# Kernel tuning notes

Hardware: AMD Instinct MI355X
Metric: run time of the kernel (lower is better)

## Reference

```python
import jax, jax.numpy as jnp
import numpy as np

# db8 decomposition low-pass filter (pywt ordering, dec_lo)
_DB8_DEC_LO = np.array([
    -0.00011747678400228192, 0.0006754494059985568, -0.0003917403729959771,
    -0.00487035299301066, 0.008746094047015655, 0.013981027917015516,
    -0.04408825393106472, -0.01736930100202211, 0.128747426620186,
    0.00047248457399797254, -0.2840155429624281, -0.015829105256023893,
    0.5853546836548691, 0.6756307362980128, 0.3128715909144659,
    0.05441584224308161], dtype=np.float32)
_F = len(_DB8_DEC_LO)  # 16 taps
# quadrature mirror relation used by pywt: dec_hi[k] = (-1)^(k+1) * dec_lo[F-1-k]
_DB8_DEC_HI = (((-1.0) ** (np.arange(_F) + 1)) * _DB8_DEC_LO[::-1]).astype(np.float32)
# lax conv is cross-correlation; np.convolve flips the kernel -> pre-flip filters.
# Kernel layout [out_ch=2 (lo,hi), in_ch=1, width=F]
_KERNEL = jnp.asarray(np.stack([_DB8_DEC_LO[::-1], _DB8_DEC_HI[::-1]])[:, None, :])

WAVELET_LEVEL = 3
SPECTRAL_WEIGHT = 1.0
WAVELET_WEIGHT = 1.0


def _dwt_level(x):
    """Single-level db8 DWT with pywt 'symmetric' padding, batched over rows.

    x: [N, L] -> (cA, cD) each [N, (L + F - 1) // 2]
    Matches: np.convolve(sym_pad(x, F-1), dec_filter, 'valid')[1::2]
    """
    p = _F - 1
    # half-sample symmetric extension: [x_p..x_1 | x | x_{L-1}..x_{L-p}]
    xe = jnp.concatenate([x[:, :p][:, ::-1], x, x[:, -p:][:, ::-1]], axis=1)
    xe = xe[:, 1:]  # start at odd offset to mimic pywt's [1::2] downsampling
    out = jax.lax.conv_general_dilated(
        xe[:, None, :], _KERNEL, window_strides=(2,), padding='VALID')  # [N,2,Lc]
    return out[:, 0, :], out[:, 1, :]


def _wavelet_loss(output, target, level):
    """Batched equivalent of the per-row pywt.wavedec loop: MSE on detail
    subbands at every level, averaged over (rows x levels)."""
    b, c, H, W = output.shape
    x = output.reshape(b * c * H, W)
    y = target.reshape(b * c * H, W)
    total = jnp.float32(0.0)
    for _ in range(level):  # fixed small loop over decomposition levels
        x, dx = _dwt_level(x)
        y, dy = _dwt_level(y)
        total = total + jnp.mean((dx - dy) ** 2)
    return total / level


def setup_inputs() -> dict:
    key = jax.random.key(0)
    k1, k2 = jax.random.split(key)
    shape = (32, 1, 1024, 1024)
    output = jax.random.normal(k1, shape, dtype=jnp.float32)
    target = jax.random.normal(k2, shape, dtype=jnp.float32)
    return {"output": output, "target": target}


def reference(output, target):
    # MSE term
    mse = jnp.mean((output - target) ** 2)
    # spectral second-difference smoothness along wavelength axis (last dim)
    sd = output[:, :, :, 2:] - 2.0 * output[:, :, :, 1:-1] + output[:, :, :, :-2]
    spectral = jnp.mean(sd ** 2)
    # original wavelet loss detaches inputs (numpy path) -> no gradient
    wavelet = _wavelet_loss(jax.lax.stop_gradient(output),
                            jax.lax.stop_gradient(target), WAVELET_LEVEL)
    return mse + SPECTRAL_WEIGHT * spectral + WAVELET_WEIGHT * wavelet
```

## Files before the change

kernel.cpp:

```cpp
#include <hip/hip_runtime.h>

#define NROWS 32768
#define NBLK  2048
#define RPW   4

typedef _Float16 h2 __attribute__((ext_vector_type(2)));

#define H2C(a,b) {(_Float16)(a##f), (_Float16)(b##f)}

__device__ __forceinline__ float DOT2(unsigned w, h2 f, float acc) {
#if __has_builtin(__builtin_amdgcn_fdot2)
    return __builtin_amdgcn_fdot2(__builtin_bit_cast(h2, w), f, acc, false);
#else
    h2 v = __builtin_bit_cast(h2, w);
    return fmaf((float)v.y, (float)f.y, fmaf((float)v.x, (float)f.x, acc));
#endif
}

__device__ __forceinline__ unsigned PK(float lo, float hi) {
    return __builtin_bit_cast(unsigned, __builtin_amdgcn_cvt_pkrtz(lo, hi));
}

__device__ __forceinline__ unsigned ROR16(unsigned v) { return (v >> 16) | (v << 16); }

__device__ __forceinline__ void wave_lgkm0() {
    asm volatile("s_waitcnt lgkmcnt(0)" ::: "memory");
}

template<int M, bool STORE>
__device__ __forceinline__ float level_group(const unsigned* __restrict__ inb,
                                             unsigned* __restrict__ outb, int g)
{
    constexpr h2 FA[8] = {
        H2C(0.05441584224308161, 0.3128715909144659),
        H2C(0.6756307362980128, 0.5853546836548691),
        H2C(-0.015829105256023893, -0.2840155429624281),
        H2C(0.00047248457399797254, 0.128747426620186),
        H2C(-0.01736930100202211, -0.04408825393106472),
        H2C(0.013981027917015516, 0.008746094047015655),
        H2C(-0.00487035299301066, -0.0003917403729959771),
        H2C(0.0006754494059985568, -0.00011747678400228192)
    };
    constexpr h2 FD[8] = {
        H2C(-0.00011747678400228192, -0.0006754494059985568),
        H2C(-0.0003917403729959771, 0.00487035299301066),
        H2C(0.008746094047015655, -0.013981027917015516),
        H2C(-0.04408825393106472, 0.01736930100202211),
        H2C(0.128747426620186, -0.00047248457399797254),
        H2C(-0.2840155429624281, 0.015829105256023893),
        H2C(0.5853546836548691, -0.6756307362980128),
        H2C(0.3128715909144659, -0.05441584224308161)
    };
    const uint4 q0 = *(const uint4*)(inb + 4 * g);
    const uint4 q1 = *(const uint4*)(inb + 4 * g + 4);
    const uint4 q2 = *(const uint4*)(inb + 4 * g + 8);
    const unsigned w[12] = {q0.x,q0.y,q0.z,q0.w, q1.x,q1.y,q1.z,q1.w, q2.x,q2.y,q2.z,q2.w};

    float aj[4] = {0.f,0.f,0.f,0.f}, dj[4] = {0.f,0.f,0.f,0.f};
#pragma unroll
    for (int c = 0; c < 8; ++c) {
#pragma unroll
        for (int j = 0; j < 4; ++j) {
            aj[j] = DOT2(w[j+1+c], FA[c], aj[j]);
            dj[j] = DOT2(w[j+1+c], FD[c], dj[j]);
        }
    }
    const int i0 = 4 * g;
    float ds = dj[0] * dj[0];
    if (i0 + 1 < M) ds += dj[1] * dj[1];
    if (i0 + 2 < M) ds += dj[2] * dj[2];
    if (i0 + 3 < M) ds += dj[3] * dj[3];
    if (STORE) {
        *(uint2*)(outb + 8 + 2 * g) = make_uint2(PK(aj[0], aj[1]), PK(aj[2], aj[3]));
    }
    return ds;
}

__device__ __forceinline__ void fix_front(unsigned* b, int l) {
    if ((unsigned)l < 7u) b[7 - l] = ROR16(b[8 + l]);
}
__device__ __forceinline__ void fix_tail_even(unsigned* b, int l, int HL) {
    if ((unsigned)l < 7u) b[8 + HL + l] = ROR16(b[8 + HL - 1 - l]);
}
__device__ __forceinline__ void fix_tail_odd(unsigned* b, int l, int q) {
    if ((unsigned)l < 7u) b[8 + q + 1 + l] = ROR16(b[8 + q - 1 - l]);
    if (l == 7) { unsigned v = b[8 + q]; b[8 + q] = (v & 0xffffu) | (v << 16); }
}

__device__ __forceinline__ float spectral_row(const float4* xc, int lane) {
    float s = 0.f;
#pragma unroll
    for (int c = 0; c < 4; ++c) {
        const float4 xv = xc[c];
        float n0 = __shfl_down(xv.x, 1, 64);
        float n1 = __shfl_down(xv.y, 1, 64);
        if (c < 3) {
            const float b0 = __shfl(xc[c + 1].x, 0, 64);
            const float b1 = __shfl(xc[c + 1].y, 0, 64);
            if (lane == 63) { n0 = b0; n1 = b1; }
        }
        const float sd0 = xv.x - 2.f * xv.y + xv.z;
        const float sd1 = xv.y - 2.f * xv.z + xv.w;
        s += sd0 * sd0 + sd1 * sd1;
        const float sd2 = xv.z - 2.f * xv.w + n0;
        const float sd3 = xv.w - 2.f * n0 + n1;
        if (c < 3 || lane < 63)
            s += sd2 * sd2 + sd3 * sd3;
    }
    return s;
}

__global__ __launch_bounds__(256) void combined_loss_kernel(
    const float* __restrict__ x, const float* __restrict__ y,
    float* __restrict__ partials)
{
    __shared__ __align__(16) unsigned lds[4][956];
    __shared__ float wsum[4];

    const int tid  = threadIdx.x;
    const int wid  = tid >> 6;
    const int lane = tid & 63;
    unsigned* const W  = lds[wid];
    unsigned* const B0 = W;
    unsigned* const B1 = W + 528;
    unsigned* const B2 = W + 804;

    const int rbase = (blockIdx.x * 4 + wid) * RPW;
    const float4* xp = (const float4*)x + (size_t)rbase * 256;
    const float4* yp = (const float4*)y + (size_t)rbase * 256;

    float4 xc[4], yc[4];
#pragma unroll
    for (int c = 0; c < 4; ++c) {
        xc[c] = xp[c * 64 + lane];
        yc[c] = yp[c * 64 + lane];
    }

    float s_mse = 0.f, s_spec = 0.f, s_d1 = 0.f, s_d2 = 0.f, s_d3 = 0.f;

#pragma unroll 1
    for (int k = 0; k < RPW; ++k) {
#pragma unroll
        for (int c = 0; c < 4; ++c) {
            const int u = c * 64 + lane;
            const float4 e = make_float4(xc[c].x - yc[c].x, xc[c].y - yc[c].y,
                                         xc[c].z - yc[c].z, xc[c].w - yc[c].w);
            s_mse += e.x * e.x + e.y * e.y + e.z * e.z + e.w * e.w;
            *(uint2*)(B0 + 8 + 2 * u) = make_uint2(PK(e.x, e.y), PK(e.z, e.w));
        }
        s_spec += spectral_row(xc, lane);

        if (k + 1 < RPW) {
            const float4* xpn = xp + (size_t)(k + 1) * 256;
            const float4* ypn = yp + (size_t)(k + 1) * 256;
#pragma unroll
            for (int c = 0; c < 4; ++c) {
                xc[c] = xpn[c * 64 + lane];
                yc[c] = ypn[c * 64 + lane];
            }
        }

        wave_lgkm0();
        fix_front(B0, lane); fix_tail_even(B0, lane - 16, 512);
        wave_lgkm0();
        for (int g = lane; g < 130; g += 64) s_d1 += level_group<519, true>(B0, B1, g);
        wave_lgkm0();
        fix_front(B1, lane); fix_tail_odd(B1, lane - 16, 259);
        wave_lgkm0();
        for (int g = lane; g < 67; g += 64)  s_d2 += level_group<267, true>(B1, B2, g);
        wave_lgkm0();
        fix_front(B2, lane); fix_tail_odd(B2, lane - 16, 133);
        wave_lgkm0();
        if (lane < 36)                       s_d3 += level_group<141, false>(B2, B2, lane);
    }

    const float wm  = 1.0f / 33554432.0f;
    const float wsp = 1.0f / 33488896.0f;
    const float w1  = 1.0f / (3.0f * 17006592.0f);
    const float w2  = 1.0f / (3.0f * 8749056.0f);
    const float w3  = 1.0f / (3.0f * 4620288.0f);
    float local = wm * s_mse + wsp * s_spec + w1 * s_d1 + w2 * s_d2 + w3 * s_d3;

#pragma unroll
    for (int off = 32; off > 0; off >>= 1)
        local += __shfl_down(local, off, 64);
    if (lane == 0) wsum[wid] = local;
    __syncthreads();
    if (tid == 0) partials[blockIdx.x] = wsum[0] + wsum[1] + wsum[2] + wsum[3];
}

__global__ __launch_bounds__(256) void reduce_kernel(const float* __restrict__ partials,
                                                     int n, float* __restrict__ out)
{
    __shared__ double sm[256];
    double s = 0.0;
    for (int i = threadIdx.x; i < n; i += 256) s += (double)partials[i];
    sm[threadIdx.x] = s;
    __syncthreads();
    for (int off = 128; off > 0; off >>= 1) {
        if (threadIdx.x < off) sm[threadIdx.x] += sm[threadIdx.x + off];
        __syncthreads();
    }
    if (threadIdx.x == 0) out[0] = (float)sm[0];
}

extern "C" void kernel_launch(void* const* d_in, const int* in_sizes, int n_in,
                              void* d_out, int out_size, void* d_ws, size_t ws_size,
                              hipStream_t stream) {
    const float* x = (const float*)d_in[0];
    const float* y = (const float*)d_in[1];
    float* partials = (float*)d_ws;
    combined_loss_kernel<<<NBLK, 256, 0, stream>>>(x, y, partials);
    reduce_kernel<<<1, 256, 0, stream>>>(partials, NBLK, (float*)d_out);
}
```

Before: 54.29 us.

## Compute 8 outputs per lane with swizzled LDS and fused boundary padding

```diff
diff --git a/kernel.cpp b/kernel.cpp
--- a/kernel.cpp
+++ b/kernel.cpp
@@ -27,9 +27,17 @@
     asm volatile("s_waitcnt lgkmcnt(0)" ::: "memory");
 }
 
+__device__ __forceinline__ unsigned pc_chunk(unsigned c) { return c ^ ((c >> 3) & 7u); }
+__device__ __forceinline__ unsigned swz32(unsigned i) {
+    return (pc_chunk(i >> 2) << 2) | (i & 3u);
+}
+__device__ __forceinline__ uint4 ldc(const unsigned* __restrict__ b, unsigned c) {
+    return ((const uint4*)b)[pc_chunk(c)];
+}
+
 template<int M, bool STORE>
-__device__ __forceinline__ float level_group(const unsigned* __restrict__ inb,
-                                             unsigned* __restrict__ outb, int g)
+__device__ __forceinline__ float level8(const unsigned* __restrict__ IB,
+                                        unsigned* __restrict__ OB, int lane)
 {
     constexpr h2 FA[8] = {
         H2C(0.05441584224308161, 0.3128715909144659),
@@ -51,40 +59,73 @@
         H2C(0.5853546836548691, -0.6756307362980128),
         H2C(0.3128715909144659, -0.05441584224308161)
     };
-    const uint4 q0 = *(const uint4*)(inb + 4 * g);
-    const uint4 q1 = *(const uint4*)(inb + 4 * g + 4);
-    const uint4 q2 = *(const uint4*)(inb + 4 * g + 8);
-    const unsigned w[12] = {q0.x,q0.y,q0.z,q0.w, q1.x,q1.y,q1.z,q1.w, q2.x,q2.y,q2.z,q2.w};
-
-    float aj[4] = {0.f,0.f,0.f,0.f}, dj[4] = {0.f,0.f,0.f,0.f};
-#pragma unroll
-    for (int c = 0; c < 8; ++c) {
-#pragma unroll
-        for (int j = 0; j < 4; ++j) {
-            aj[j] = DOT2(w[j+1+c], FA[c], aj[j]);
-            dj[j] = DOT2(w[j+1+c], FD[c], dj[j]);
-        }
-    }
-    const int i0 = 4 * g;
-    float ds = dj[0] * dj[0];
-    if (i0 + 1 < M) ds += dj[1] * dj[1];
-    if (i0 + 2 < M) ds += dj[2] * dj[2];
-    if (i0 + 3 < M) ds += dj[3] * dj[3];
-    if (STORE) {
-        *(uint2*)(outb + 8 + 2 * g) = make_uint2(PK(aj[0], aj[1]), PK(aj[2], aj[3]));
+    constexpr int G    = M / 8;
+    constexpr int TAIL = M - 8 * G;
+    constexpr int q    = (M - 1) / 2;
+    float ds = 0.f;
+
+    if (lane < G) {
+        const uint4 c0 = ldc(IB, 2*lane+0), c1 = ldc(IB, 2*lane+1),
+                    c2 = ldc(IB, 2*lane+2), c3 = ldc(IB, 2*lane+3);
+        const unsigned w[16] = {c0.x,c0.y,c0.z,c0.w, c1.x,c1.y,c1.z,c1.w,
+                                c2.x,c2.y,c2.z,c2.w, c3.x,c3.y,c3.z,c3.w};
+        float a[8] = {0,0,0,0,0,0,0,0}, d[8] = {0,0,0,0,0,0,0,0};
+#pragma unroll
+        for (int c = 0; c < 8; ++c) {
+#pragma unroll
+            for (int j = 0; j < 8; ++j) {
+                if constexpr (STORE) a[j] = DOT2(w[j+1+c], FA[c], a[j]);
+                d[j] = DOT2(w[j+1+c], FD[c], d[j]);
+            }
+        }
+#pragma unroll
+        for (int j = 0; j < 8; ++j) ds += d[j] * d[j];
+        if constexpr (STORE) {
+            unsigned P[4];
+#pragma unroll
+            for (int t = 0; t < 4; ++t) P[t] = PK(a[2*t], a[2*t+1]);
+            ((uint4*)OB)[pc_chunk(2 + lane)] = make_uint4(P[0], P[1], P[2], P[3]);
+#pragma unroll
+            for (int t = 0; t < 4; ++t) {
+                const int p = 4 * lane + t;
+                if (p <= 6)                   OB[swz32(7 - p)]       = ROR16(P[t]);
+                if (p >= q - 7 && p <= q - 1) OB[swz32(8 + 2*q - p)] = ROR16(P[t]);
+            }
+        }
+    }
+    if (lane == 0) {
+        const uint4 c0 = ldc(IB, 2*G+0), c1 = ldc(IB, 2*G+1),
+                    c2 = ldc(IB, 2*G+2), c3 = ldc(IB, 2*G+3);
+        const unsigned w[16] = {c0.x,c0.y,c0.z,c0.w, c1.x,c1.y,c1.z,c1.w,
+                                c2.x,c2.y,c2.z,c2.w, c3.x,c3.y,c3.z,c3.w};
+        float a[8] = {0,0,0,0,0,0,0,0};
+#pragma unroll
+        for (int t = 0; t < TAIL; ++t) {
+            float at = 0.f, dt = 0.f;
+#pragma unroll
+            for (int c = 0; c < 8; ++c) {
+                if constexpr (STORE) at = DOT2(w[t+1+c], FA[c], at);
+                dt = DOT2(w[t+1+c], FD[c], dt);
+            }
+            ds += dt * dt;
+            a[t] = at;
+        }
+        if constexpr (STORE) {
+            if constexpr (TAIL == 7) {
+                const unsigned P0 = PK(a[0], a[1]), P1 = PK(a[2], a[3]),
+                               P2 = PK(a[4], a[5]), P3 = PK(a[6], a[6]);
+                ((uint4*)OB)[pc_chunk(2 + G)] = make_uint4(P0, P1, P2, P3);
+                OB[swz32(8 + 2*q - (4*G + 0))] = ROR16(P0);
+                OB[swz32(8 + 2*q - (4*G + 1))] = ROR16(P1);
+                OB[swz32(8 + 2*q - (4*G + 2))] = ROR16(P2);
+            } else {
+                const unsigned P0 = PK(a[0], a[1]), P1 = PK(a[2], a[2]);
+                *(uint2*)(OB + swz32(8 + 4*G)) = make_uint2(P0, P1);
+                OB[swz32(8 + 2*q - 4*G)] = ROR16(P0);
+            }
+        }
     }
     return ds;
-}
-
-__device__ __forceinline__ void fix_front(unsigned* b, int l) {
-    if ((unsigned)l < 7u) b[7 - l] = ROR16(b[8 + l]);
-}
-__device__ __forceinline__ void fix_tail_even(unsigned* b, int l, int HL) {
-    if ((unsigned)l < 7u) b[8 + HL + l] = ROR16(b[8 + HL - 1 - l]);
-}
-__device__ __forceinline__ void fix_tail_odd(unsigned* b, int l, int q) {
-    if ((unsigned)l < 7u) b[8 + q + 1 + l] = ROR16(b[8 + q - 1 - l]);
-    if (l == 7) { unsigned v = b[8 + q]; b[8 + q] = (v & 0xffffu) | (v << 16); }
 }
 
 __device__ __forceinline__ float spectral_row(const float4* xc, int lane) {
@@ -114,7 +155,7 @@
     const float* __restrict__ x, const float* __restrict__ y,
     float* __restrict__ partials)
 {
-    __shared__ __align__(16) unsigned lds[4][956];
+    __shared__ __align__(16) unsigned lds[4][964];
     __shared__ float wsum[4];
 
     const int tid  = threadIdx.x;
@@ -146,40 +187,41 @@
             const float4 e = make_float4(xc[c].x - yc[c].x, xc[c].y - yc[c].y,
                                          xc[c].z - yc[c].z, xc[c].w - yc[c].w);
             s_mse += e.x * e.x + e.y * e.y + e.z * e.z + e.w * e.w;
-            *(uint2*)(B0 + 8 + 2 * u) = make_uint2(PK(e.x, e.y), PK(e.z, e.w));
+            *(uint2*)(B0 + swz32(8 + 2 * u)) = make_uint2(PK(e.x, e.y), PK(e.z, e.w));
+            if (c == 0 && lane <= 3) {
+                B0[swz32(7 - 2 * lane)] = PK(e.y, e.x);
+                if (lane <= 2) B0[swz32(6 - 2 * lane)] = PK(e.w, e.z);
+            }
+            if (c == 3 && lane >= 60) {
+                if (lane >= 61) B0[swz32(1031 - 2 * u)] = PK(e.y, e.x);
+                B0[swz32(1030 - 2 * u)] = PK(e.w, e.z);
+            }
         }
         s_spec += spectral_row(xc, lane);
 
         if (k + 1 < RPW) {
+            const float4* ypn = yp + (size_t)(k + 1) * 256;
             const float4* xpn = xp + (size_t)(k + 1) * 256;
-            const float4* ypn = yp + (size_t)(k + 1) * 256;
-#pragma unroll
-            for (int c = 0; c < 4; ++c) {
-                xc[c] = xpn[c * 64 + lane];
-                yc[c] = ypn[c * 64 + lane];
-            }
+#pragma unroll
+            for (int c = 0; c < 4; ++c) yc[c] = ypn[c * 64 + lane];
+#pragma unroll
+            for (int c = 0; c < 4; ++c) xc[c] = xpn[c * 64 + lane];
         }
 
         wave_lgkm0();
-        fix_front(B0, lane); fix_tail_even(B0, lane - 16, 512);
+        s_d1 += level8<519, true>(B0, B1, lane);
         wave_lgkm0();
-        for (int g = lane; g < 130; g += 64) s_d1 += level_group<519, true>(B0, B1, g);
+        s_d2 += level8<267, true>(B1, B2, lane);
         wave_lgkm0();
-        fix_front(B1, lane); fix_tail_odd(B1, lane - 16, 259);
-        wave_lgkm0();
-        for (int g = lane; g < 67; g += 64)  s_d2 += level_group<267, true>(B1, B2, g);
-        wave_lgkm0();
-        fix_front(B2, lane); fix_tail_odd(B2, lane - 16, 133);
-        wave_lgkm0();
-        if (lane < 36)                       s_d3 += level_group<141, false>(B2, B2, lane);
+        s_d3 += level8<141, false>(B2, B2, lane);
     }
 
     const float wm  = 1.0f / 33554432.0f;
     const float wsp = 1.0f / 33488896.0f;
-    const float w1  = 1.0f / (3.0f * 17006592.0f);
-    const float w2  = 1.0f / (3.0f * 8749056.0f);
-    const float w3  = 1.0f / (3.0f * 4620288.0f);
-    float local = wm * s_mse + wsp * s_spec + w1 * s_d1 + w2 * s_d2 + w3 * s_d3;
+    const float w1w = 1.0f / (3.0f * 17006592.0f);
+    const float w2w = 1.0f / (3.0f * 8749056.0f);
+    const float w3w = 1.0f / (3.0f * 4620288.0f);
+    float local = wm * s_mse + wsp * s_spec + w1w * s_d1 + w2w * s_d2 + w3w * s_d3;
 
 #pragma unroll
     for (int off = 32; off > 0; off >>= 1)
```

Result: slower. 64.67 us (+19.1%).
